# Kernel tuning notes

Measured on AMD Instinct MI355X. Metric: run time of the kernel, lower is better.

## Reference

```python
import jax, jax.numpy as jnp
import numpy as np

HID = 128
IN = 28
SEQ = 28
NUM_LAYERS = 10  # num_classes mistakenly passed as num_layers in the source
NUM_CLASSES = 10


def setup_inputs() -> dict:
    key = jax.random.key(0)
    ks = jax.random.split(key, 9)
    s = 1.0 / np.sqrt(HID)  # pytorch nn.RNN init scale
    x = jax.random.normal(ks[0], (4096, SEQ, IN), dtype=jnp.float32)
    W_ih0 = jax.random.uniform(ks[1], (HID, IN), jnp.float32, -s, s)
    W_ih = jax.random.uniform(ks[2], (NUM_LAYERS - 1, HID, HID), jnp.float32, -s, s)
    W_hh = jax.random.uniform(ks[3], (NUM_LAYERS, HID, HID), jnp.float32, -s, s)
    b_ih = jax.random.uniform(ks[4], (NUM_LAYERS, HID), jnp.float32, -s, s)
    b_hh = jax.random.uniform(ks[5], (NUM_LAYERS, HID), jnp.float32, -s, s)
    fc_W = jax.random.uniform(ks[6], (NUM_CLASSES, HID), jnp.float32, -s, s)
    fc_b = jax.random.uniform(ks[7], (NUM_CLASSES,), jnp.float32, -s, s)
    return {"x": x, "W_ih0": W_ih0, "W_ih": W_ih, "W_hh": W_hh,
            "b_ih": b_ih, "b_hh": b_hh, "fc_W": fc_W, "fc_b": fc_b}


def _rnn_layer(xs, Wih, Whh, bih, bhh):
    # xs: [B, T, F]; precompute the input projection once (batched GEMM),
    # then scan only the recurrent matmul + tanh.
    B = xs.shape[0]
    xp = jnp.einsum('btf,hf->bth', xs, Wih) + bih + bhh  # [B, T, H]

    def step(h, xp_t):
        h = jnp.tanh(xp_t + h @ Whh.T)
        return h, h

    h0 = jnp.zeros((B, Whh.shape[0]), xs.dtype)
    _, ys = jax.lax.scan(step, h0, jnp.swapaxes(xp, 0, 1))  # [T, B, H]
    return jnp.swapaxes(ys, 0, 1)  # [B, T, H]


def reference(x, W_ih0, W_ih, W_hh, b_ih, b_hh, fc_W, fc_b):
    x = x.reshape(-1, SEQ, IN)
    h = _rnn_layer(x, W_ih0, W_hh[0], b_ih[0], b_hh[0])
    for l in range(1, NUM_LAYERS):
        h = _rnn_layer(h, W_ih[l - 1], W_hh[l], b_ih[l], b_hh[l])
    # fc on last timestep
    return h[:, -1, :] @ fc_W.T + fc_b
```

## Files before the change

kernel.cpp:

```cpp
#include <hip/hip_runtime.h>
#include <cstdint>
#include <cstddef>

#define HID 128
#define SEQL 28
#define INP 28
#define NL 10
#define NC 10
#define BATCH 4096
#define BB 16
#define STRD 136
#define BUFH (16 * STRD)

typedef _Float16 half8 __attribute__((ext_vector_type(8)));
typedef _Float16 half4 __attribute__((ext_vector_type(4)));
typedef float    f32x4 __attribute__((ext_vector_type(4)));

#define WS_WCAT_OFF 0
#define WS_BIAS_OFF 655360
#define WS_SEQ_OFF  660480

__global__ void convert_weights(const float* __restrict__ Wih0,
                                const float* __restrict__ Wih,
                                const float* __restrict__ Whh,
                                const float* __restrict__ bih,
                                const float* __restrict__ bhh,
                                _Float16* __restrict__ Wcat,
                                float* __restrict__ bias) {
  int tg = blockIdx.x * blockDim.x + threadIdx.x;
  if (tg >= NL * HID * 16) return;
  int r = tg >> 4, seg = tg & 15;
  int l = r / HID, n = r % HID;
  int k0 = seg * 16;
  _Float16* dst = Wcat + (size_t)r * 256 + k0;
  if (l == 0) {
#pragma unroll
    for (int i = 0; i < 16; ++i) {
      int k = k0 + i;
      float v = 0.f;
      if (k < INP) v = Wih0[n * INP + k];
      else if (k >= HID) v = Whh[(size_t)n * HID + (k - HID)];
      dst[i] = (_Float16)v;
    }
  } else {
    const float* src = (k0 < HID)
        ? (Wih + ((size_t)(l - 1) * HID + n) * HID + k0)
        : (Whh + ((size_t)l * HID + n) * HID + (k0 - HID));
#pragma unroll
    for (int i = 0; i < 16; ++i) dst[i] = (_Float16)src[i];
  }
  if (seg == 0) bias[r] = bih[r] + bhh[r];
}

__device__ __forceinline__ float tanh_fast(float v) {
  float e = __builtin_amdgcn_exp2f(v * 2.8853900817779268f);
  float r = __builtin_amdgcn_rcpf(e + 1.f);
  return __builtin_fmaf(-2.f, r, 1.f);
}

__device__ __forceinline__ void barrier_light() {
  __builtin_amdgcn_sched_barrier(0);
  asm volatile("s_waitcnt lgkmcnt(0)" ::: "memory");
  __builtin_amdgcn_s_barrier();
  __builtin_amdgcn_sched_barrier(0);
}

__global__ __launch_bounds__(512, 2) void rnn_fused(
    const float* __restrict__ x,
    const _Float16* __restrict__ Wcat,
    const float* __restrict__ bias,
    const float* __restrict__ fcW,
    const float* __restrict__ fcb,
    _Float16* __restrict__ seq,
    float* __restrict__ out) {
  __shared__ _Float16 lds[BUFH * 10] __attribute__((aligned(16)));

  const int tid    = threadIdx.x;
  const int lane15 = tid & 15;
  const int quad   = (tid >> 4) & 3;
  const int wid    = tid >> 6;
  const int s      = wid >> 1;
  const int nhalf  = wid & 1;
  const int n0     = nhalf * 64;
  const int b0     = blockIdx.x * BB;
  const int frow1  = tid >> 5;
  const int fseg1  = tid & 31;
  const int frow0  = tid >> 3;
  const int fc0    = (tid & 7) * 4;

  const int rdoff = lane15 * STRD + quad * 8;
  const int wroff = lane15 * STRD + n0 + quad * 4;

  half8 wf[4][8];
  f32x4 bias4[4];

  for (int g = 0; g < 3; ++g) {
    const int L = g * 4 + s;
    if (L < NL) {
      const _Float16* Wl = Wcat + (size_t)L * HID * 256;
#pragma unroll
      for (int nn = 0; nn < 4; ++nn) {
#pragma unroll
        for (int ks = 0; ks < 8; ++ks)
          wf[nn][ks] = *(const half8*)(Wl + (size_t)(n0 + nn * 16 + lane15) * 256 + ks * 32 + quad * 8);
        bias4[nn] = *(const f32x4*)(bias + L * HID + n0 + nn * 16 + quad * 4);
      }
    }
    __syncthreads();
    {
      uint4 z; z.x = z.y = z.z = z.w = 0u;
      for (int i = tid; i < (BUFH * 8) / 8; i += 512)
        ((uint4*)(lds + 2 * BUFH))[i] = z;
    }

    f32x4 pfx[2];
    uint2 pfu[2];

    auto load_next = [&](int t, int sl) {
      if (g == 0) {
        if (tid < 128) {
          const float* xb = x + ((size_t)(b0 + frow0) * SEQL + t) * INP;
          if (fc0 < INP) pfx[sl] = *(const f32x4*)(xb + fc0);
          else { f32x4 z4 = {0.f, 0.f, 0.f, 0.f}; pfx[sl] = z4; }
        }
      } else {
        pfu[sl] = *(const uint2*)(seq + ((size_t)(b0 + frow1) * SEQL + t) * HID + fseg1 * 4);
      }
    };
    auto store_X = [&](int sl) {
      if (g == 0) {
        if (tid < 128) {
          _Float16 h4[4];
#pragma unroll
          for (int i = 0; i < 4; ++i) h4[i] = (_Float16)pfx[sl][i];
          *(uint2*)(lds + sl * BUFH + frow0 * STRD + fc0) = *(const uint2*)h4;
        }
      } else {
        *(uint2*)(lds + sl * BUFH + frow1 * STRD + fseg1 * 4) = pfu[sl];
      }
    };

    load_next(0, 0);
    store_X(0);
    load_next(1, 1);

    auto tick = [&](int tau, int pt) {
      barrier_light();
      if (tau + 2 < SEQL) load_next(tau + 2, pt);
      const int t = tau - s;
      if (L < NL && (unsigned)t < SEQL) {
        const _Float16* INb = (s == 0) ? lds + pt * BUFH
                                       : lds + (2 + 2 * (s - 1) + (1 - pt)) * BUFH;
        const _Float16* Hb  = lds + (2 + 2 * s + (1 - pt)) * BUFH;
        _Float16*       Ob  = lds + (2 + 2 * s + pt) * BUFH;
        const bool wseq = (g < 2) && (s == 3);

        auto tw = [&](int nn, f32x4 av) {
          half4 o;
#pragma unroll
          for (int r = 0; r < 4; ++r) o[r] = (_Float16)tanh_fast(av[r]);
          *(half4*)(Ob + wroff + nn * 16) = o;
          if (wseq)
            *(half4*)(seq + ((size_t)(b0 + lane15) * SEQL + t) * HID + n0 + nn * 16 + quad * 4) = o;
        };

        if (g == 0 && s == 0) {
          half8 ax = *(const half8*)(INb + rdoff);
          half8 ah[4];
#pragma unroll
          for (int ks = 0; ks < 4; ++ks) ah[ks] = *(const half8*)(Hb + rdoff + ks * 32);
          f32x4 a0 = bias4[0], a1 = bias4[1];
          a0 = __builtin_amdgcn_mfma_f32_16x16x32_f16(wf[0][0], ax, a0, 0, 0, 0);
          a1 = __builtin_amdgcn_mfma_f32_16x16x32_f16(wf[1][0], ax, a1, 0, 0, 0);
#pragma unroll
          for (int ks = 0; ks < 4; ++ks) {
            a0 = __builtin_amdgcn_mfma_f32_16x16x32_f16(wf[0][4 + ks], ah[ks], a0, 0, 0, 0);
            a1 = __builtin_amdgcn_mfma_f32_16x16x32_f16(wf[1][4 + ks], ah[ks], a1, 0, 0, 0);
          }
          f32x4 a2 = bias4[2], a3 = bias4[3];
          a2 = __builtin_amdgcn_mfma_f32_16x16x32_f16(wf[2][0], ax, a2, 0, 0, 0);
          a3 = __builtin_amdgcn_mfma_f32_16x16x32_f16(wf[3][0], ax, a3, 0, 0, 0);
#pragma unroll
          for (int ks = 0; ks < 4; ++ks) {
            a2 = __builtin_amdgcn_mfma_f32_16x16x32_f16(wf[2][4 + ks], ah[ks], a2, 0, 0, 0);
            a3 = __builtin_amdgcn_mfma_f32_16x16x32_f16(wf[3][4 + ks], ah[ks], a3, 0, 0, 0);
          }
          tw(0, a0); tw(1, a1); tw(2, a2); tw(3, a3);
        } else {
          half8 af[8];
#pragma unroll
          for (int ks = 0; ks < 4; ++ks) af[ks] = *(const half8*)(INb + rdoff + ks * 32);
#pragma unroll
          for (int ks = 0; ks < 4; ++ks) af[4 + ks] = *(const half8*)(Hb + rdoff + ks * 32);
          f32x4 a0 = bias4[0], a1 = bias4[1];
#pragma unroll
          for (int i = 0; i < 8; ++i) {
            a0 = __builtin_amdgcn_mfma_f32_16x16x32_f16(wf[0][i], af[i], a0, 0, 0, 0);
            a1 = __builtin_amdgcn_mfma_f32_16x16x32_f16(wf[1][i], af[i], a1, 0, 0, 0);
          }
          f32x4 a2 = bias4[2], a3 = bias4[3];
#pragma unroll
          for (int i = 0; i < 8; ++i) {
            a2 = __builtin_amdgcn_mfma_f32_16x16x32_f16(wf[2][i], af[i], a2, 0, 0, 0);
            a3 = __builtin_amdgcn_mfma_f32_16x16x32_f16(wf[3][i], af[i], a3, 0, 0, 0);
          }
          tw(0, a0); tw(1, a1); tw(2, a2); tw(3, a3);
        }
      }
      if (tau + 1 < SEQL) store_X(1 - pt);
    };

    const int Tend = (g == 2) ? 28 : 30;
    for (int tau = 0; tau < Tend; tau += 2) {
      tick(tau, 0);
      tick(tau + 1, 1);
    }
    tick(Tend, 0);
  }
  __syncthreads();

  if (tid < BB * NC) {
    int c = tid >> 4;
    int b = tid & 15;
    float acc = fcb[c];
    const float* wr = fcW + c * HID;
    const _Float16* hr = lds + BUFH * 4 + b * STRD;
#pragma unroll
    for (int k0 = 0; k0 < HID; k0 += 8) {
      half8 h = *(const half8*)(hr + k0);
      f32x4 w0 = *(const f32x4*)(wr + k0);
      f32x4 w1 = *(const f32x4*)(wr + k0 + 4);
#pragma unroll
      for (int j = 0; j < 4; ++j)
        acc += (float)h[j] * w0[j] + (float)h[j + 4] * w1[j];
    }
    out[(size_t)(b0 + b) * NC + c] = acc;
  }
}

extern "C" void kernel_launch(void* const* d_in, const int* in_sizes, int n_in,
                              void* d_out, int out_size, void* d_ws, size_t ws_size,
                              hipStream_t stream) {
  const float* x    = (const float*)d_in[0];
  const float* Wih0 = (const float*)d_in[1];
  const float* Wih  = (const float*)d_in[2];
  const float* Whh  = (const float*)d_in[3];
  const float* bih  = (const float*)d_in[4];
  const float* bhh  = (const float*)d_in[5];
  const float* fcW  = (const float*)d_in[6];
  const float* fcb  = (const float*)d_in[7];
  float* out = (float*)d_out;

  _Float16* Wcat = (_Float16*)((char*)d_ws + WS_WCAT_OFF);
  float*    bs   = (float*)((char*)d_ws + WS_BIAS_OFF);
  _Float16* seq  = (_Float16*)((char*)d_ws + WS_SEQ_OFF);

  convert_weights<<<dim3(80), dim3(256), 0, stream>>>(Wih0, Wih, Whh, bih, bhh, Wcat, bs);
  rnn_fused<<<dim3(BATCH / BB), dim3(512), 0, stream>>>(x, Wcat, bs, fcW, fcb, seq, out);
}
```

Before: 205.8 us.

## Keep inter-group layer outputs in LDS instead of global workspace

The full 28-step output sequence of the last layer in each 4-layer group now stays in dynamic LDS (28 extra slots) rather than being written to and re-read from a global seq buffer. The next group's first layer reads its input directly from those slots. This removes global stores and loads, plus their prefetch logic, for layer groups after the first. The cost is about 157 KiB of LDS per block, which limits each CU to one block, and it requires a dynamic shared memory attribute.

```diff
diff --git a/kernel.cpp b/kernel.cpp
--- a/kernel.cpp
+++ b/kernel.cpp
@@ -12,13 +12,15 @@
 #define STRD 136
 #define BUFH (16 * STRD)
 
+#define NSLOT 37
+#define LDS_BYTES (NSLOT * BUFH * 2)
+
 typedef _Float16 half8 __attribute__((ext_vector_type(8)));
 typedef _Float16 half4 __attribute__((ext_vector_type(4)));
 typedef float    f32x4 __attribute__((ext_vector_type(4)));
 
 #define WS_WCAT_OFF 0
 #define WS_BIAS_OFF 655360
-#define WS_SEQ_OFF  660480
 
 __global__ void convert_weights(const float* __restrict__ Wih0,
                                 const float* __restrict__ Wih,
@@ -71,9 +73,8 @@
     const float* __restrict__ bias,
     const float* __restrict__ fcW,
     const float* __restrict__ fcb,
-    _Float16* __restrict__ seq,
     float* __restrict__ out) {
-  __shared__ _Float16 lds[BUFH * 10] __attribute__((aligned(16)));
+  extern __shared__ __align__(16) _Float16 lds[];
 
   const int tid    = threadIdx.x;
   const int lane15 = tid & 15;
@@ -83,8 +84,6 @@
   const int nhalf  = wid & 1;
   const int n0     = nhalf * 64;
   const int b0     = blockIdx.x * BB;
-  const int frow1  = tid >> 5;
-  const int fseg1  = tid & 31;
   const int frow0  = tid >> 3;
   const int fc0    = (tid & 7) * 4;
 
@@ -109,59 +108,53 @@
     __syncthreads();
     {
       uint4 z; z.x = z.y = z.z = z.w = 0u;
-      for (int i = tid; i < (BUFH * 8) / 8; i += 512)
+      for (int i = tid; i < (BUFH * 7) / 8; i += 512)
         ((uint4*)(lds + 2 * BUFH))[i] = z;
     }
 
     f32x4 pfx[2];
-    uint2 pfu[2];
 
     auto load_next = [&](int t, int sl) {
-      if (g == 0) {
-        if (tid < 128) {
-          const float* xb = x + ((size_t)(b0 + frow0) * SEQL + t) * INP;
-          if (fc0 < INP) pfx[sl] = *(const f32x4*)(xb + fc0);
-          else { f32x4 z4 = {0.f, 0.f, 0.f, 0.f}; pfx[sl] = z4; }
-        }
-      } else {
-        pfu[sl] = *(const uint2*)(seq + ((size_t)(b0 + frow1) * SEQL + t) * HID + fseg1 * 4);
+      if (tid < 128) {
+        const float* xb = x + ((size_t)(b0 + frow0) * SEQL + t) * INP;
+        if (fc0 < INP) pfx[sl] = *(const f32x4*)(xb + fc0);
+        else { f32x4 z4 = {0.f, 0.f, 0.f, 0.f}; pfx[sl] = z4; }
       }
     };
     auto store_X = [&](int sl) {
-      if (g == 0) {
-        if (tid < 128) {
-          _Float16 h4[4];
-#pragma unroll
-          for (int i = 0; i < 4; ++i) h4[i] = (_Float16)pfx[sl][i];
-          *(uint2*)(lds + sl * BUFH + frow0 * STRD + fc0) = *(const uint2*)h4;
-        }
-      } else {
-        *(uint2*)(lds + sl * BUFH + frow1 * STRD + fseg1 * 4) = pfu[sl];
+      if (tid < 128) {
+        _Float16 h4[4];
+#pragma unroll
+        for (int i = 0; i < 4; ++i) h4[i] = (_Float16)pfx[sl][i];
+        *(uint2*)(lds + sl * BUFH + frow0 * STRD + fc0) = *(const uint2*)h4;
       }
     };
 
-    load_next(0, 0);
-    store_X(0);
-    load_next(1, 1);
+    if (g == 0) {
+      load_next(0, 0);
+      store_X(0);
+      load_next(1, 1);
+    }
 
     auto tick = [&](int tau, int pt) {
       barrier_light();
-      if (tau + 2 < SEQL) load_next(tau + 2, pt);
+      if (g == 0 && tau + 2 < SEQL) load_next(tau + 2, pt);
       const int t = tau - s;
       if (L < NL && (unsigned)t < SEQL) {
-        const _Float16* INb = (s == 0) ? lds + pt * BUFH
-                                       : lds + (2 + 2 * (s - 1) + (1 - pt)) * BUFH;
-        const _Float16* Hb  = lds + (2 + 2 * s + (1 - pt)) * BUFH;
-        _Float16*       Ob  = lds + (2 + 2 * s + pt) * BUFH;
-        const bool wseq = (g < 2) && (s == 3);
+        const _Float16* INb;
+        if (s == 0) INb = (g == 0) ? lds + pt * BUFH : lds + (9 + t) * BUFH;
+        else        INb = lds + (2 + 2 * (s - 1) + (1 - pt)) * BUFH;
+        const _Float16* Hb = (s == 3)
+            ? ((t == 0) ? lds + 8 * BUFH : lds + (9 + (t - 1)) * BUFH)
+            : lds + (2 + 2 * s + (1 - pt)) * BUFH;
+        _Float16* Ob = (s == 3) ? lds + (9 + t) * BUFH
+                                : lds + (2 + 2 * s + pt) * BUFH;
 
         auto tw = [&](int nn, f32x4 av) {
           half4 o;
 #pragma unroll
           for (int r = 0; r < 4; ++r) o[r] = (_Float16)tanh_fast(av[r]);
           *(half4*)(Ob + wroff + nn * 16) = o;
-          if (wseq)
-            *(half4*)(seq + ((size_t)(b0 + lane15) * SEQL + t) * HID + n0 + nn * 16 + quad * 4) = o;
         };
 
         if (g == 0 && s == 0) {
@@ -207,7 +200,7 @@
           tw(0, a0); tw(1, a1); tw(2, a2); tw(3, a3);
         }
       }
-      if (tau + 1 < SEQL) store_X(1 - pt);
+      if (g == 0 && tau + 1 < SEQL) store_X(1 - pt);
     };
 
     const int Tend = (g == 2) ? 28 : 30;
@@ -253,8 +246,14 @@
 
   _Float16* Wcat = (_Float16*)((char*)d_ws + WS_WCAT_OFF);
   float*    bs   = (float*)((char*)d_ws + WS_BIAS_OFF);
-  _Float16* seq  = (_Float16*)((char*)d_ws + WS_SEQ_OFF);
+
+  static bool attr_done = false;
+  if (!attr_done) {
+    hipFuncSetAttribute(reinterpret_cast<const void*>(rnn_fused),
+                        hipFuncAttributeMaxDynamicSharedMemorySize, LDS_BYTES);
+    attr_done = true;
+  }
 
   convert_weights<<<dim3(80), dim3(256), 0, stream>>>(Wih0, Wih, Whh, bih, bhh, Wcat, bs);
-  rnn_fused<<<dim3(BATCH / BB), dim3(512), 0, stream>>>(x, Wcat, bs, fcW, fcb, seq, out);
-}
+  rnn_fused<<<dim3(BATCH / BB), dim3(512), LDS_BYTES, stream>>>(x, Wcat, bs, fcW, fcb, out);
+}
```

New measurement: 180.5 us. 1.14x faster.
